# Performance work log

Measured on AMD Instinct MI355X. Metric: run time of the kernel, lower is better.

## Reference

```python
import jax, jax.numpy as jnp
import numpy as np

N = 100000   # nodes
S = 2        # layout samples per graph
G = 8        # graphs in batch
E = 400000   # directed edges
MID = 256    # mid_ch
L = 4        # n_layer
CLN = 2      # concat_last_n
IN_CH = 53 + 32 + 6 * 23 + 6 * 3 + 6 * 4  # 265


def setup_inputs() -> dict:
    key = jax.random.key(0)
    ks = jax.random.split(key, 16)
    f = lambda k, sh: jax.random.normal(k, sh, dtype=jnp.float32)
    return {
        "x_feat": f(ks[0], (N, 53)),
        "dim_feat": f(ks[1], (N, 6, 23)),
        "layout_feat": f(ks[2], (N, S, 6, 4)),
        "tile_feat": f(ks[3], (G, S, 6, 3)),
        "opcode_embed": f(ks[4], (121, 32)) * 0.02,
        "preW": f(ks[5], (IN_CH, MID)) * 0.05,
        "preb": jnp.zeros((MID,), jnp.float32),
        "convWl": f(ks[6], (L, MID, MID // 2)) * 0.05,
        "convWr": f(ks[7], (L, MID, MID // 2)) * 0.05,
        "convb": jnp.zeros((L, MID // 2), jnp.float32),
        "revWl": f(ks[8], (L, MID, MID // 2)) * 0.05,
        "revWr": f(ks[9], (L, MID, MID // 2)) * 0.05,
        "revb": jnp.zeros((L, MID // 2), jnp.float32),
        "headW": f(ks[10], (MID * CLN, 1)) * 0.05,
        "headb": jnp.zeros((1,), jnp.float32),
        "node_opcode": jax.random.randint(ks[11], (N,), 0, 121),
        "batch": jnp.sort(jax.random.randint(ks[12], (N,), 0, G)),
        "edge_index": jax.random.randint(ks[13], (2, E), 0, N),
    }


def _sage(x, src, tgt, inv_deg, Wl, Wr, b):
    # PyG SAGEConv: out = lin_l(mean_{j->i} x_j) + lin_r(x_i) + bias
    # x: [S, N, C]; gather messages from src, scatter-add into tgt.
    agg = jnp.zeros_like(x).at[:, tgt].add(x[:, src])
    agg = agg * inv_deg[None, :, None]
    return (jnp.einsum('snc,co->sno', agg, Wl)
            + jnp.einsum('snc,co->sno', x, Wr) + b)


def reference(x_feat, dim_feat, layout_feat, tile_feat, opcode_embed,
              preW, preb, convWl, convWr, convb, revWl, revWr, revb,
              headW, headb, node_opcode, batch, edge_index):
    op = opcode_embed[node_opcode]                       # [N, 32]
    base = jnp.concatenate([x_feat, op, dim_feat.reshape(N, -1)], axis=-1)
    x = jnp.concatenate([
        jnp.broadcast_to(base[None], (S,) + base.shape),          # [S,N,223]
        layout_feat.transpose(1, 0, 2, 3).reshape(S, N, -1),       # [S,N,24]
        tile_feat[batch].transpose(1, 0, 2, 3).reshape(S, N, -1),  # [S,N,18]
    ], axis=-1)                                                    # [S,N,265]
    x = jax.nn.relu(x @ preW + preb)                               # [S,N,MID]

    src, tgt = edge_index[0], edge_index[1]
    one = jnp.ones((E,), x.dtype)
    inv_fwd = 1.0 / jnp.maximum(jnp.zeros((N,), x.dtype).at[tgt].add(one), 1.0)
    inv_rev = 1.0 / jnp.maximum(jnp.zeros((N,), x.dtype).at[src].add(one), 1.0)

    xs = []
    for i in range(L):
        x = jnp.concatenate([
            _sage(x, src, tgt, inv_fwd, convWl[i], convWr[i], convb[i]),
            _sage(x, tgt, src, inv_rev, revWl[i], revWr[i], revb[i]),
        ], axis=-1)
        x = jax.nn.relu(x)
        if i >= L - CLN:
            xs.append(x)
    x = jnp.concatenate(xs, axis=-1)                     # [S, N, MID*CLN]

    pooled = jnp.zeros((S, G, x.shape[-1]), x.dtype).at[:, batch].add(x)
    out = pooled @ headW + headb                         # [S, G, 1]
    return out.transpose(1, 0, 2)                        # [G, S, 1]
```

## Files before the change

kernel.cpp:

```cpp
#include <hip/hip_runtime.h>
#include <hip/hip_bf16.h>

#define N_NODES 100000
#define S_SAMP 2
#define G_GRAPH 8
#define E_EDGES 400000
#define NLAYER 4
#define IN_CH 265
#define KPRE 384
#define NRT64 ((N_NODES + 63) / 64)
#define NPAD (NRT64 * 64)
#define NGRP ((NRT64 + 7) / 8)
#define NB1 ((N_NODES + 1023) / 1024)

typedef unsigned short u16;
typedef unsigned int u32;
typedef short bf16x8 __attribute__((ext_vector_type(8)));
typedef float f32x4 __attribute__((ext_vector_type(4)));

__device__ __forceinline__ float b2f(u16 u) {
    union { u32 i; float f; } x; x.i = ((u32)u) << 16; return x.f;
}
__device__ __forceinline__ u16 f2b(float f) {
    __hip_bfloat16 h = __float2bfloat16(f);
    return *reinterpret_cast<u16*>(&h);
}

__device__ __forceinline__ void gl_lds16(const u16* g, u16* l) {
    __builtin_amdgcn_global_load_lds(
        (const __attribute__((address_space(1))) void*)g,
        (__attribute__((address_space(3))) void*)l, 16, 0, 0);
}

__global__ void build_xin_k(const float* __restrict__ xf,
                            const float* __restrict__ dimf,
                            const float* __restrict__ layf,
                            const float* __restrict__ tilef,
                            const float* __restrict__ opemb,
                            const int* __restrict__ opcode,
                            const int* __restrict__ batch,
                            int s, u16* __restrict__ xin) {
    int n = blockIdx.x;
    int opc = opcode[n];
    int g = batch[n];
    u16* row = xin + (size_t)n * KPRE;
    for (int c = threadIdx.x; c < KPRE; c += blockDim.x) {
        float v = 0.0f;
        if (c < 53)       v = xf[(size_t)n * 53 + c];
        else if (c < 85)  v = opemb[opc * 32 + (c - 53)];
        else if (c < 223) v = dimf[(size_t)n * 138 + (c - 85)];
        else if (c < 247) v = layf[((size_t)n * S_SAMP + s) * 24 + (c - 223)];
        else if (c < 265) v = tilef[((size_t)g * S_SAMP + s) * 18 + (c - 247)];
        row[c] = f2b(v);
    }
}

__global__ void pack_w_k(const float* __restrict__ cWl, const float* __restrict__ rWl,
                         const float* __restrict__ cWr, const float* __restrict__ rWr,
                         const float* __restrict__ cb,  const float* __restrict__ rb,
                         u16* __restrict__ Wt, float* __restrict__ bcat) {
    int idx = blockIdx.x * blockDim.x + threadIdx.x;
    if (idx < NLAYER * 512 * 256) {
        int l = idx >> 17;
        int r = idx & 131071;
        int j = r >> 8;
        int k = r & 255;
        int jj = j & 255;
        int half = j >> 8;
        int sub = jj >> 7;
        int col = jj & 127;
        const float* src = half ? (sub ? rWl : cWl) : (sub ? rWr : cWr);
        Wt[idx] = f2b(src[((size_t)l * 256 + k) * 128 + col]);
    }
    if (idx < NLAYER * 512) {
        int l = idx >> 9;
        int j = idx & 511;
        float v = 0.0f;
        if (j < 256) v = (j < 128) ? cb[l * 128 + j] : rb[l * 128 + (j - 128)];
        bcat[idx] = v;
    }
}

__global__ void pack_pre_k(const float* __restrict__ preW, u16* __restrict__ preWt) {
    int idx = blockIdx.x * blockDim.x + threadIdx.x;
    if (idx >= 256 * KPRE) return;
    int j = idx / KPRE;
    int k = idx - j * KPRE;
    preWt[idx] = (k < IN_CH) ? f2b(preW[(size_t)k * 256 + j]) : (u16)0;
}

__global__ void deg_k(const int* __restrict__ ei, int* __restrict__ degF,
                      int* __restrict__ degR) {
    int e = blockIdx.x * blockDim.x + threadIdx.x;
    if (e < E_EDGES) {
        atomicAdd(&degF[ei[E_EDGES + e]], 1);
        atomicAdd(&degR[ei[e]], 1);
    }
}

__global__ __launch_bounds__(1024) void scan1_k(const int* __restrict__ degF,
                                                const int* __restrict__ degR,
                                                int* __restrict__ rpF,
                                                int* __restrict__ rpR,
                                                int* __restrict__ bsum) {
    const int* deg = blockIdx.y ? degR : degF;
    int* rp = blockIdx.y ? rpR : rpF;
    __shared__ int buf[1024];
    int i = blockIdx.x * 1024 + threadIdx.x;
    int v = (i < N_NODES) ? deg[i] : 0;
    buf[threadIdx.x] = v;
    __syncthreads();
    for (int off = 1; off < 1024; off <<= 1) {
        int t = (threadIdx.x >= off) ? buf[threadIdx.x - off] : 0;
        __syncthreads();
        buf[threadIdx.x] += t;
        __syncthreads();
    }
    if (i < N_NODES) rp[i] = buf[threadIdx.x] - v;
    if (threadIdx.x == 1023) bsum[blockIdx.y * NB1 + blockIdx.x] = buf[1023];
}

__global__ __launch_bounds__(256) void scan2_k(int* __restrict__ bsum,
                                               int* __restrict__ rpF,
                                               int* __restrict__ rpR) {
    __shared__ int buf[2][128];
    int half = threadIdx.x >> 7;
    int t = threadIdx.x & 127;
    int v = (t < NB1) ? bsum[half * NB1 + t] : 0;
    buf[half][t] = v;
    __syncthreads();
    for (int off = 1; off < 128; off <<= 1) {
        int x = (t >= off) ? buf[half][t - off] : 0;
        __syncthreads();
        buf[half][t] += x;
        __syncthreads();
    }
    if (t < NB1) bsum[half * NB1 + t] = buf[half][t] - v;
    if (t == NB1) (half ? rpR : rpF)[N_NODES] = buf[half][NB1 - 1];
}

__global__ void scan3_k(const int* __restrict__ bsum, int* __restrict__ rpF,
                        int* __restrict__ rpR) {
    int* rp = blockIdx.y ? rpR : rpF;
    int i = blockIdx.x * 1024 + threadIdx.x;
    if (i < N_NODES) rp[i] += bsum[blockIdx.y * NB1 + blockIdx.x];
}

__global__ void inv_cursor_k(const int* __restrict__ degF, const int* __restrict__ degR,
                             const int* __restrict__ rpF, const int* __restrict__ rpR,
                             float* __restrict__ invF, float* __restrict__ invR,
                             int* __restrict__ curF, int* __restrict__ curR) {
    int i = blockIdx.x * blockDim.x + threadIdx.x;
    if (i < N_NODES) {
        invF[i] = 1.0f / fmaxf((float)degF[i], 1.0f);
        invR[i] = 1.0f / fmaxf((float)degR[i], 1.0f);
        curF[i] = rpF[i];
        curR[i] = rpR[i];
    }
}

__global__ void fill_k(const int* __restrict__ ei, int* __restrict__ curF,
                       int* __restrict__ curR, int* __restrict__ colF,
                       int* __restrict__ colR) {
    int e = blockIdx.x * blockDim.x + threadIdx.x;
    if (e < E_EDGES) {
        int s = ei[e], t = ei[E_EDGES + e];
        colF[atomicAdd(&curF[t], 1)] = s;
        colR[atomicAdd(&curR[s], 1)] = t;
    }
}

template <bool RELU_OUT, int NCHUNK, int COLT>
__global__ __launch_bounds__(256) void mmA_k(const u16* __restrict__ A,
                                             const u16* __restrict__ Bt,
                                             const float* __restrict__ bias,
                                             u16* __restrict__ C0,
                                             u16* __restrict__ C1) {
    __shared__ u16 As[64 * 128];
    __shared__ u16 Bs[64 * 128];
    constexpr int K = NCHUNK * 128;

    int bid = blockIdx.x;
    int x = bid & 7;
    int q = bid >> 3;
    int c = q % COLT;
    int g = q / COLT;
    int rowTile = g * 8 + x;
    if (rowTile >= NRT64) return;
    int rowBase = rowTile * 64;
    int colBase = c * 64;

    int tid = threadIdx.x;
    int wv = tid >> 6;
    int lane = tid & 63;
    int quad = lane >> 4;
    int l16 = lane & 15;

    int rsub = lane >> 4;
    int sl = lane & 15;

    f32x4 acc[4] = {};

    for (int ci = 0; ci < NCHUNK; ci++) {
        int k0 = ci * 128;
        #pragma unroll
        for (int i = 0; i < 4; i++) {
            int r = wv * 16 + 4 * i + rsub;
            int ch = sl ^ (r & 15);
            gl_lds16(A + (size_t)(rowBase + r) * K + k0 + ch * 8,
                     As + (wv * 16 + 4 * i) * 128);
            gl_lds16(Bt + (size_t)(colBase + r) * K + k0 + ch * 8,
                     Bs + (wv * 16 + 4 * i) * 128);
        }
        __syncthreads();
        int ra = wv * 16 + l16;
        #pragma unroll
        for (int ks = 0; ks < 4; ks++) {
            int ca = ks * 4 + quad;
            bf16x8 af = *(const bf16x8*)(As + ra * 128 + (ca ^ (ra & 15)) * 8);
            #pragma unroll
            for (int cf = 0; cf < 4; cf++) {
                int rb = cf * 16 + l16;
                bf16x8 bf = *(const bf16x8*)(Bs + rb * 128 + (ca ^ (rb & 15)) * 8);
                acc[cf] = __builtin_amdgcn_mfma_f32_16x16x32_bf16(af, bf, acc[cf], 0, 0, 0);
            }
        }
        if (ci + 1 < NCHUNK) __syncthreads();
    }

    u16* dst = (colBase < 256) ? C0 : C1;
    int cb = colBase & 255;
    #pragma unroll
    for (int cf = 0; cf < 4; cf++) {
        int col = cb + cf * 16 + l16;
        float bv = bias[colBase + cf * 16 + l16];
        #pragma unroll
        for (int r = 0; r < 4; r++) {
            int row = rowBase + wv * 16 + quad * 4 + r;
            if (row < N_NODES) {
                float v = acc[cf][r] + bv;
                if (RELU_OUT) v = fmaxf(v, 0.0f);
                dst[(size_t)row * 256 + col] = f2b(v);
            }
        }
    }
}

template <bool DOT>
__global__ __launch_bounds__(256) void agg_k(const int* __restrict__ rpF,
                                             const int* __restrict__ colF,
                                             const int* __restrict__ rpR,
                                             const int* __restrict__ colR,
                                             const float* __restrict__ invF,
                                             const float* __restrict__ invR,
                                             const u16* __restrict__ H,
                                             u16* __restrict__ Xn,
                                             const float* __restrict__ w,
                                             float* __restrict__ dotbuf) {
    int n = (blockIdx.x * blockDim.x + threadIdx.x) >> 6;
    if (n >= N_NODES) return;
    int lane = threadIdx.x & 63;
    int half = lane >> 5;
    int l32 = lane & 31;
    const int* rp  = half ? rpR : rpF;
    const int* col = half ? colR : colF;
    float inv = half ? invR[n] : invF[n];
    const u16* Hb = H + half * 128 + 4 * l32;

    float a0 = 0, a1 = 0, a2 = 0, a3 = 0;
    int b = rp[n], e = rp[n + 1];
    int j = b;
    for (; j + 7 < e; j += 8) {
        int c0 = col[j],     c1 = col[j + 1], c2 = col[j + 2], c3 = col[j + 3];
        int c4 = col[j + 4], c5 = col[j + 5], c6 = col[j + 6], c7 = col[j + 7];
        ushort4 h0 = *(const ushort4*)(Hb + (size_t)c0 * 256);
        ushort4 h1 = *(const ushort4*)(Hb + (size_t)c1 * 256);
        ushort4 h2 = *(const ushort4*)(Hb + (size_t)c2 * 256);
        ushort4 h3 = *(const ushort4*)(Hb + (size_t)c3 * 256);
        ushort4 h4 = *(const ushort4*)(Hb + (size_t)c4 * 256);
        ushort4 h5 = *(const ushort4*)(Hb + (size_t)c5 * 256);
        ushort4 h6 = *(const ushort4*)(Hb + (size_t)c6 * 256);
        ushort4 h7 = *(const ushort4*)(Hb + (size_t)c7 * 256);
        a0 += b2f(h0.x) + b2f(h1.x) + b2f(h2.x) + b2f(h3.x)
            + b2f(h4.x) + b2f(h5.x) + b2f(h6.x) + b2f(h7.x);
        a1 += b2f(h0.y) + b2f(h1.y) + b2f(h2.y) + b2f(h3.y)
            + b2f(h4.y) + b2f(h5.y) + b2f(h6.y) + b2f(h7.y);
        a2 += b2f(h0.z) + b2f(h1.z) + b2f(h2.z) + b2f(h3.z)
            + b2f(h4.z) + b2f(h5.z) + b2f(h6.z) + b2f(h7.z);
        a3 += b2f(h0.w) + b2f(h1.w) + b2f(h2.w) + b2f(h3.w)
            + b2f(h4.w) + b2f(h5.w) + b2f(h6.w) + b2f(h7.w);
    }
    for (; j + 3 < e; j += 4) {
        int c0 = col[j], c1 = col[j + 1], c2 = col[j + 2], c3 = col[j + 3];
        ushort4 h0 = *(const ushort4*)(Hb + (size_t)c0 * 256);
        ushort4 h1 = *(const ushort4*)(Hb + (size_t)c1 * 256);
        ushort4 h2 = *(const ushort4*)(Hb + (size_t)c2 * 256);
        ushort4 h3 = *(const ushort4*)(Hb + (size_t)c3 * 256);
        a0 += b2f(h0.x) + b2f(h1.x) + b2f(h2.x) + b2f(h3.x);
        a1 += b2f(h0.y) + b2f(h1.y) + b2f(h2.y) + b2f(h3.y);
        a2 += b2f(h0.z) + b2f(h1.z) + b2f(h2.z) + b2f(h3.z);
        a3 += b2f(h0.w) + b2f(h1.w) + b2f(h2.w) + b2f(h3.w);
    }
    for (; j < e; j++) {
        int c = col[j];
        ushort4 h = *(const ushort4*)(Hb + (size_t)c * 256);
        a0 += b2f(h.x); a1 += b2f(h.y); a2 += b2f(h.z); a3 += b2f(h.w);
    }
    u16* xp = Xn + (size_t)n * 256 + 4 * lane;
    ushort4 xv = *(const ushort4*)xp;
    float v0 = fmaxf(b2f(xv.x) + a0 * inv, 0.0f);
    float v1 = fmaxf(b2f(xv.y) + a1 * inv, 0.0f);
    float v2 = fmaxf(b2f(xv.z) + a2 * inv, 0.0f);
    float v3 = fmaxf(b2f(xv.w) + a3 * inv, 0.0f);
    ushort4 o;
    o.x = f2b(v0); o.y = f2b(v1); o.z = f2b(v2); o.w = f2b(v3);
    *(ushort4*)xp = o;
    if (DOT) {
        float4 wv4 = *(const float4*)(w + 4 * lane);
        float d = v0 * wv4.x + v1 * wv4.y + v2 * wv4.z + v3 * wv4.w;
        #pragma unroll
        for (int off = 32; off > 0; off >>= 1) d += __shfl_down(d, off);
        if (lane == 0) dotbuf[n] = d;
    }
}

__global__ void out_init_k(float* __restrict__ out, const float* __restrict__ headb) {
    int i = threadIdx.x;
    if (i < G_GRAPH * S_SAMP) out[i] = headb[0];
}

__global__ __launch_bounds__(256) void reduce_k(const float* __restrict__ dotbuf,
                                                const int* __restrict__ batch,
                                                float* __restrict__ out, int s) {
    __shared__ float part[G_GRAPH];
    if (threadIdx.x < G_GRAPH) part[threadIdx.x] = 0.0f;
    __syncthreads();
    for (int i = blockIdx.x * 256 + threadIdx.x; i < N_NODES; i += gridDim.x * 256)
        atomicAdd(&part[batch[i]], dotbuf[i]);
    __syncthreads();
    if (threadIdx.x < G_GRAPH)
        atomicAdd(&out[threadIdx.x * S_SAMP + s], part[threadIdx.x]);
}

extern "C" void kernel_launch(void* const* d_in, const int* in_sizes, int n_in,
                              void* d_out, int out_size, void* d_ws, size_t ws_size,
                              hipStream_t stream) {
    const float* x_feat      = (const float*)d_in[0];
    const float* dim_feat    = (const float*)d_in[1];
    const float* layout_feat = (const float*)d_in[2];
    const float* tile_feat   = (const float*)d_in[3];
    const float* opemb       = (const float*)d_in[4];
    const float* preW        = (const float*)d_in[5];
    const float* preb        = (const float*)d_in[6];
    const float* convWl      = (const float*)d_in[7];
    const float* convWr      = (const float*)d_in[8];
    const float* convb       = (const float*)d_in[9];
    const float* revWl       = (const float*)d_in[10];
    const float* revWr       = (const float*)d_in[11];
    const float* revb        = (const float*)d_in[12];
    const float* headW       = (const float*)d_in[13];
    const float* headb       = (const float*)d_in[14];
    const int*   node_opcode = (const int*)d_in[15];
    const int*   batch       = (const int*)d_in[16];
    const int*   edge_index  = (const int*)d_in[17];
    float* out = (float*)d_out;

    char* ws = (char*)d_ws;
    size_t off = 0;
    auto alloc = [&](size_t nbytes) {
        char* p = ws + off;
        off += (nbytes + 255) & ~(size_t)255;
        return p;
    };
    u16* XA    = (u16*)alloc((size_t)NPAD * 256 * 2);
    u16* XB    = (u16*)alloc((size_t)NPAD * 256 * 2);
    u16* XinH  = (u16*)alloc((size_t)NPAD * KPRE * 2);
    u16* Wt    = (u16*)alloc((size_t)NLAYER * 512 * 256 * 2);
    u16* preWt = (u16*)alloc((size_t)256 * KPRE * 2);
    float* bcat = (float*)alloc(NLAYER * 512 * 4);
    float* dotbuf = (float*)alloc((size_t)N_NODES * 4);
    int* degF  = (int*)alloc(N_NODES * 4);
    int* degR  = (int*)alloc(N_NODES * 4);
    int* rpF   = (int*)alloc((N_NODES + 1) * 4);
    int* rpR   = (int*)alloc((N_NODES + 1) * 4);
    int* curF  = (int*)alloc(N_NODES * 4);
    int* curR  = (int*)alloc(N_NODES * 4);
    int* colF  = (int*)alloc(E_EDGES * 4);
    int* colR  = (int*)alloc(E_EDGES * 4);
    int* bsum  = (int*)alloc(2 * NB1 * 4);
    float* invF = (float*)alloc(N_NODES * 4);
    float* invR = (float*)alloc(N_NODES * 4);

    hipMemsetAsync(degF, 0, N_NODES * 4, stream);
    hipMemsetAsync(degR, 0, N_NODES * 4, stream);

    pack_w_k<<<(NLAYER * 512 * 256 + 255) / 256, 256, 0, stream>>>(
        convWl, revWl, convWr, revWr, convb, revb, Wt, bcat);
    pack_pre_k<<<(256 * KPRE + 255) / 256, 256, 0, stream>>>(preW, preWt);
    deg_k<<<(E_EDGES + 255) / 256, 256, 0, stream>>>(edge_index, degF, degR);
    scan1_k<<<dim3(NB1, 2), 1024, 0, stream>>>(degF, degR, rpF, rpR, bsum);
    scan2_k<<<1, 256, 0, stream>>>(bsum, rpF, rpR);
    scan3_k<<<dim3(NB1, 2), 1024, 0, stream>>>(bsum, rpF, rpR);
    inv_cursor_k<<<(N_NODES + 255) / 256, 256, 0, stream>>>(
        degF, degR, rpF, rpR, invF, invR, curF, curR);
    fill_k<<<(E_EDGES + 255) / 256, 256, 0, stream>>>(edge_index, curF, curR, colF, colR);

    out_init_k<<<1, 64, 0, stream>>>(out, headb);

    for (int s = 0; s < S_SAMP; s++) {
        build_xin_k<<<N_NODES, 256, 0, stream>>>(
            x_feat, dim_feat, layout_feat, tile_feat, opemb, node_opcode, batch, s, XinH);
        mmA_k<true, 3, 4><<<NGRP * 8 * 4, 256, 0, stream>>>(
            XinH, preWt, preb, XA, XA);

        u16* ins[NLAYER]  = {XA, XB, XA, XB};
        u16* outs[NLAYER] = {XB, XA, XB, XA};
        for (int l = 0; l < NLAYER; l++) {
            mmA_k<false, 2, 8><<<NGRP * 8 * 8, 256, 0, stream>>>(
                ins[l], Wt + (size_t)l * 512 * 256, bcat + (size_t)l * 512,
                outs[l], XinH);
            if (l < 2) {
                agg_k<false><<<(N_NODES * 64 + 255) / 256, 256, 0, stream>>>(
                    rpF, colF, rpR, colR, invF, invR, XinH, outs[l], nullptr, nullptr);
            } else {
                agg_k<true><<<(N_NODES * 64 + 255) / 256, 256, 0, stream>>>(
                    rpF, colF, rpR, colR, invF, invR, XinH, outs[l],
                    headW + (l == 2 ? 0 : 256), dotbuf);
                reduce_k<<<128, 256, 0, stream>>>(dotbuf, batch, out, s);
            }
        }
    }
}
```

Before: 1.504 ms.

## Merge both layout samples into single batched GEMM and aggregation passes

When the workspace is large enough, both samples are processed together. One input build writes the shared features plus each sample's layout and tile columns. A single pre-GEMM with 512 output columns uses a repacked weight so each column half yields one sample. All layer GEMMs, aggregations and reductions then run over 2N rows, halving the kernel launches and letting the graph gather reuse CSR reads across samples. The input build kernels are also vectorised to write four values per thread. The cost is more workspace, and the merged path only runs if ws_size reaches 330MB; otherwise the old per-sample path runs.

```diff
diff --git a/kernel.cpp b/kernel.cpp
--- a/kernel.cpp
+++ b/kernel.cpp
@@ -10,8 +10,9 @@
 #define KPRE 384
 #define NRT64 ((N_NODES + 63) / 64)
 #define NPAD (NRT64 * 64)
-#define NGRP ((NRT64 + 7) / 8)
 #define NB1 ((N_NODES + 1023) / 1024)
+#define M2 (S_SAMP * N_NODES)
+#define MT2 (M2 / 64)
 
 typedef unsigned short u16;
 typedef unsigned int u32;
@@ -32,27 +33,66 @@
         (__attribute__((address_space(3))) void*)l, 16, 0, 0);
 }
 
-__global__ void build_xin_k(const float* __restrict__ xf,
-                            const float* __restrict__ dimf,
-                            const float* __restrict__ layf,
-                            const float* __restrict__ tilef,
-                            const float* __restrict__ opemb,
-                            const int* __restrict__ opcode,
-                            const int* __restrict__ batch,
-                            int s, u16* __restrict__ xin) {
-    int n = blockIdx.x;
+__global__ __launch_bounds__(256) void build_m_k(const float* __restrict__ xf,
+                                                 const float* __restrict__ dimf,
+                                                 const float* __restrict__ layf,
+                                                 const float* __restrict__ tilef,
+                                                 const float* __restrict__ opemb,
+                                                 const int* __restrict__ opcode,
+                                                 const int* __restrict__ batch,
+                                                 u16* __restrict__ A2) {
+    int item = blockIdx.x * blockDim.x + threadIdx.x;
+    int n = item / 77;
+    if (n >= N_NODES) return;
+    int base = (item - n * 77) * 4;
     int opc = opcode[n];
     int g = batch[n];
-    u16* row = xin + (size_t)n * KPRE;
-    for (int c = threadIdx.x; c < KPRE; c += blockDim.x) {
+    ushort4 o;
+    u16* op = &o.x;
+    #pragma unroll
+    for (int u = 0; u < 4; u++) {
+        int c = base + u;
         float v = 0.0f;
         if (c < 53)       v = xf[(size_t)n * 53 + c];
         else if (c < 85)  v = opemb[opc * 32 + (c - 53)];
         else if (c < 223) v = dimf[(size_t)n * 138 + (c - 85)];
-        else if (c < 247) v = layf[((size_t)n * S_SAMP + s) * 24 + (c - 223)];
-        else if (c < 265) v = tilef[((size_t)g * S_SAMP + s) * 18 + (c - 247)];
-        row[c] = f2b(v);
-    }
+        else if (c < 247) v = layf[((size_t)n * 2 + 0) * 24 + (c - 223)];
+        else if (c < 265) v = tilef[((size_t)g * 2 + 0) * 18 + (c - 247)];
+        else if (c < 289) v = layf[((size_t)n * 2 + 1) * 24 + (c - 265)];
+        else if (c < 307) v = tilef[((size_t)g * 2 + 1) * 18 + (c - 289)];
+        op[u] = f2b(v);
+    }
+    *(ushort4*)(A2 + (size_t)n * KPRE + base) = o;
+}
+
+__global__ __launch_bounds__(256) void build_s_k(const float* __restrict__ xf,
+                                                 const float* __restrict__ dimf,
+                                                 const float* __restrict__ layf,
+                                                 const float* __restrict__ tilef,
+                                                 const float* __restrict__ opemb,
+                                                 const int* __restrict__ opcode,
+                                                 const int* __restrict__ batch,
+                                                 int s, u16* __restrict__ xin) {
+    int item = blockIdx.x * blockDim.x + threadIdx.x;
+    int n = item / 67;
+    if (n >= N_NODES) return;
+    int base = (item - n * 67) * 4;
+    int opc = opcode[n];
+    int g = batch[n];
+    ushort4 o;
+    u16* op = &o.x;
+    #pragma unroll
+    for (int u = 0; u < 4; u++) {
+        int c = base + u;
+        float v = 0.0f;
+        if (c < 53)       v = xf[(size_t)n * 53 + c];
+        else if (c < 85)  v = opemb[opc * 32 + (c - 53)];
+        else if (c < 223) v = dimf[(size_t)n * 138 + (c - 85)];
+        else if (c < 247) v = layf[((size_t)n * 2 + s) * 24 + (c - 223)];
+        else if (c < 265) v = tilef[((size_t)g * 2 + s) * 18 + (c - 247)];
+        op[u] = f2b(v);
+    }
+    *(ushort4*)(xin + (size_t)n * KPRE + base) = o;
 }
 
 __global__ void pack_w_k(const float* __restrict__ cWl, const float* __restrict__ rWl,
@@ -87,6 +127,26 @@
     int j = idx / KPRE;
     int k = idx - j * KPRE;
     preWt[idx] = (k < IN_CH) ? f2b(preW[(size_t)k * 256 + j]) : (u16)0;
+}
+
+__global__ void pack_pre2_k(const float* __restrict__ preW,
+                            const float* __restrict__ preb,
+                            u16* __restrict__ W2t, float* __restrict__ bias2) {
+    int idx = blockIdx.x * blockDim.x + threadIdx.x;
+    if (idx < 512 * KPRE) {
+        int j = idx / KPRE;
+        int k = idx - j * KPRE;
+        float v = 0.0f;
+        if (j < 256) {
+            if (k < IN_CH) v = preW[(size_t)k * 256 + j];
+        } else {
+            int jj = j - 256;
+            if (k < 223) v = preW[(size_t)k * 256 + jj];
+            else if (k >= 265 && k < 307) v = preW[(size_t)(k - 42) * 256 + jj];
+        }
+        W2t[idx] = f2b(v);
+    }
+    if (idx < 512) bias2[idx] = preb[idx & 255];
 }
 
 __global__ void deg_k(const int* __restrict__ ei, int* __restrict__ degF,
@@ -175,7 +235,8 @@
                                              const u16* __restrict__ Bt,
                                              const float* __restrict__ bias,
                                              u16* __restrict__ C0,
-                                             u16* __restrict__ C1) {
+                                             u16* __restrict__ C1,
+                                             int M, int Mtiles) {
     __shared__ u16 As[64 * 128];
     __shared__ u16 Bs[64 * 128];
     constexpr int K = NCHUNK * 128;
@@ -186,7 +247,7 @@
     int c = q % COLT;
     int g = q / COLT;
     int rowTile = g * 8 + x;
-    if (rowTile >= NRT64) return;
+    if (rowTile >= Mtiles) return;
     int rowBase = rowTile * 64;
     int colBase = c * 64;
 
@@ -195,7 +256,6 @@
     int lane = tid & 63;
     int quad = lane >> 4;
     int l16 = lane & 15;
-
     int rsub = lane >> 4;
     int sl = lane & 15;
 
@@ -237,7 +297,7 @@
         #pragma unroll
         for (int r = 0; r < 4; r++) {
             int row = rowBase + wv * 16 + quad * 4 + r;
-            if (row < N_NODES) {
+            if (row < M) {
                 float v = acc[cf][r] + bv;
                 if (RELU_OUT) v = fmaxf(v, 0.0f);
                 dst[(size_t)row * 256 + col] = f2b(v);
@@ -256,16 +316,19 @@
                                              const u16* __restrict__ H,
                                              u16* __restrict__ Xn,
                                              const float* __restrict__ w,
-                                             float* __restrict__ dotbuf) {
-    int n = (blockIdx.x * blockDim.x + threadIdx.x) >> 6;
-    if (n >= N_NODES) return;
+                                             float* __restrict__ dotbuf,
+                                             int nodes) {
+    int i = (blockIdx.x * blockDim.x + threadIdx.x) >> 6;
+    if (i >= nodes) return;
+    int s = (i >= N_NODES) ? 1 : 0;
+    int n = i - s * N_NODES;
     int lane = threadIdx.x & 63;
     int half = lane >> 5;
     int l32 = lane & 31;
     const int* rp  = half ? rpR : rpF;
     const int* col = half ? colR : colF;
     float inv = half ? invR[n] : invF[n];
-    const u16* Hb = H + half * 128 + 4 * l32;
+    const u16* Hb = H + ((size_t)s * N_NODES) * 256 + half * 128 + 4 * l32;
 
     float a0 = 0, a1 = 0, a2 = 0, a3 = 0;
     int b = rp[n], e = rp[n + 1];
@@ -306,7 +369,7 @@
         ushort4 h = *(const ushort4*)(Hb + (size_t)c * 256);
         a0 += b2f(h.x); a1 += b2f(h.y); a2 += b2f(h.z); a3 += b2f(h.w);
     }
-    u16* xp = Xn + (size_t)n * 256 + 4 * lane;
+    u16* xp = Xn + (size_t)i * 256 + 4 * lane;
     ushort4 xv = *(const ushort4*)xp;
     float v0 = fmaxf(b2f(xv.x) + a0 * inv, 0.0f);
     float v1 = fmaxf(b2f(xv.y) + a1 * inv, 0.0f);
@@ -320,7 +383,7 @@
         float d = v0 * wv4.x + v1 * wv4.y + v2 * wv4.z + v3 * wv4.w;
         #pragma unroll
         for (int off = 32; off > 0; off >>= 1) d += __shfl_down(d, off);
-        if (lane == 0) dotbuf[n] = d;
+        if (lane == 0) dotbuf[i] = d;
     }
 }
 
@@ -331,15 +394,19 @@
 
 __global__ __launch_bounds__(256) void reduce_k(const float* __restrict__ dotbuf,
                                                 const int* __restrict__ batch,
-                                                float* __restrict__ out, int s) {
-    __shared__ float part[G_GRAPH];
-    if (threadIdx.x < G_GRAPH) part[threadIdx.x] = 0.0f;
+                                                float* __restrict__ out,
+                                                int count, int s_base) {
+    __shared__ float part[G_GRAPH * S_SAMP];
+    if (threadIdx.x < G_GRAPH * S_SAMP) part[threadIdx.x] = 0.0f;
     __syncthreads();
-    for (int i = blockIdx.x * 256 + threadIdx.x; i < N_NODES; i += gridDim.x * 256)
-        atomicAdd(&part[batch[i]], dotbuf[i]);
+    for (int i = blockIdx.x * 256 + threadIdx.x; i < count; i += gridDim.x * 256) {
+        int s = s_base + ((i >= N_NODES) ? 1 : 0);
+        int n = (i >= N_NODES) ? i - N_NODES : i;
+        atomicAdd(&part[batch[n] * S_SAMP + s], dotbuf[i]);
+    }
     __syncthreads();
-    if (threadIdx.x < G_GRAPH)
-        atomicAdd(&out[threadIdx.x * S_SAMP + s], part[threadIdx.x]);
+    if (threadIdx.x < G_GRAPH * S_SAMP)
+        atomicAdd(&out[threadIdx.x], part[threadIdx.x]);
 }
 
 extern "C" void kernel_launch(void* const* d_in, const int* in_sizes, int n_in,
@@ -365,6 +432,8 @@
     const int*   edge_index  = (const int*)d_in[17];
     float* out = (float*)d_out;
 
+    const bool merged = ws_size >= (330ull << 20);
+
     char* ws = (char*)d_ws;
     size_t off = 0;
     auto alloc = [&](size_t nbytes) {
@@ -372,13 +441,16 @@
         off += (nbytes + 255) & ~(size_t)255;
         return p;
     };
-    u16* XA    = (u16*)alloc((size_t)NPAD * 256 * 2);
-    u16* XB    = (u16*)alloc((size_t)NPAD * 256 * 2);
-    u16* XinH  = (u16*)alloc((size_t)NPAD * KPRE * 2);
+    size_t xrows = merged ? (size_t)M2 : (size_t)NPAD;
+    u16* XA   = (u16*)alloc(xrows * 256 * 2);
+    u16* XB   = (u16*)alloc(xrows * 256 * 2);
+    u16* A2H  = (u16*)alloc(merged ? (size_t)M2 * 256 * 2 : (size_t)NPAD * KPRE * 2);
     u16* Wt    = (u16*)alloc((size_t)NLAYER * 512 * 256 * 2);
     u16* preWt = (u16*)alloc((size_t)256 * KPRE * 2);
-    float* bcat = (float*)alloc(NLAYER * 512 * 4);
-    float* dotbuf = (float*)alloc((size_t)N_NODES * 4);
+    u16* W2t   = (u16*)alloc((size_t)512 * KPRE * 2);
+    float* bcat  = (float*)alloc(NLAYER * 512 * 4);
+    float* bias2 = (float*)alloc(512 * 4);
+    float* dotbuf = (float*)alloc((merged ? M2 : N_NODES) * 4);
     int* degF  = (int*)alloc(N_NODES * 4);
     int* degR  = (int*)alloc(N_NODES * 4);
     int* rpF   = (int*)alloc((N_NODES + 1) * 4);
@@ -396,7 +468,6 @@
 
     pack_w_k<<<(NLAYER * 512 * 256 + 255) / 256, 256, 0, stream>>>(
         convWl, revWl, convWr, revWr, convb, revb, Wt, bcat);
-    pack_pre_k<<<(256 * KPRE + 255) / 256, 256, 0, stream>>>(preW, preWt);
     deg_k<<<(E_EDGES + 255) / 256, 256, 0, stream>>>(edge_index, degF, degR);
     scan1_k<<<dim3(NB1, 2), 1024, 0, stream>>>(degF, degR, rpF, rpR, bsum);
     scan2_k<<<1, 256, 0, stream>>>(bsum, rpF, rpR);
@@ -404,30 +475,63 @@
     inv_cursor_k<<<(N_NODES + 255) / 256, 256, 0, stream>>>(
         degF, degR, rpF, rpR, invF, invR, curF, curR);
     fill_k<<<(E_EDGES + 255) / 256, 256, 0, stream>>>(edge_index, curF, curR, colF, colR);
-
     out_init_k<<<1, 64, 0, stream>>>(out, headb);
 
-    for (int s = 0; s < S_SAMP; s++) {
-        build_xin_k<<<N_NODES, 256, 0, stream>>>(
-            x_feat, dim_feat, layout_feat, tile_feat, opemb, node_opcode, batch, s, XinH);
-        mmA_k<true, 3, 4><<<NGRP * 8 * 4, 256, 0, stream>>>(
-            XinH, preWt, preb, XA, XA);
-
+    if (merged) {
+        pack_pre2_k<<<(512 * KPRE + 255) / 256, 256, 0, stream>>>(preW, preb, W2t, bias2);
+        build_m_k<<<(N_NODES * 77 + 255) / 256, 256, 0, stream>>>(
+            x_feat, dim_feat, layout_feat, tile_feat, opemb, node_opcode, batch, A2H);
+        const int gridPre = ((NRT64 + 7) / 8) * 8 * 8;
+        mmA_k<true, 3, 8><<<gridPre, 256, 0, stream>>>(
+            A2H, W2t, bias2, XA, XA + (size_t)N_NODES * 256, N_NODES, NRT64);
+
+        const int gridL = ((MT2 + 7) / 8) * 8 * 8;
+        const int gridAgg = (M2 * 64 + 255) / 256;
         u16* ins[NLAYER]  = {XA, XB, XA, XB};
         u16* outs[NLAYER] = {XB, XA, XB, XA};
         for (int l = 0; l < NLAYER; l++) {
-            mmA_k<false, 2, 8><<<NGRP * 8 * 8, 256, 0, stream>>>(
+            mmA_k<false, 2, 8><<<gridL, 256, 0, stream>>>(
                 ins[l], Wt + (size_t)l * 512 * 256, bcat + (size_t)l * 512,
-                outs[l], XinH);
+                outs[l], A2H, M2, MT2);
             if (l < 2) {
-                agg_k<false><<<(N_NODES * 64 + 255) / 256, 256, 0, stream>>>(
-                    rpF, colF, rpR, colR, invF, invR, XinH, outs[l], nullptr, nullptr);
+                agg_k<false><<<gridAgg, 256, 0, stream>>>(
+                    rpF, colF, rpR, colR, invF, invR, A2H, outs[l],
+                    nullptr, nullptr, M2);
             } else {
-                agg_k<true><<<(N_NODES * 64 + 255) / 256, 256, 0, stream>>>(
-                    rpF, colF, rpR, colR, invF, invR, XinH, outs[l],
-                    headW + (l == 2 ? 0 : 256), dotbuf);
-                reduce_k<<<128, 256, 0, stream>>>(dotbuf, batch, out, s);
+                agg_k<true><<<gridAgg, 256, 0, stream>>>(
+                    rpF, colF, rpR, colR, invF, invR, A2H, outs[l],
+                    headW + (l == 2 ? 0 : 256), dotbuf, M2);
+                reduce_k<<<128, 256, 0, stream>>>(dotbuf, batch, out, M2, 0);
             }
         }
-    }
-}
+    } else {
+        pack_pre_k<<<(256 * KPRE + 255) / 256, 256, 0, stream>>>(preW, preWt);
+        const int gridPre = ((NRT64 + 7) / 8) * 8 * 4;
+        const int gridL   = ((NRT64 + 7) / 8) * 8 * 8;
+        const int gridAgg = (N_NODES * 64 + 255) / 256;
+        for (int s = 0; s < S_SAMP; s++) {
+            build_s_k<<<(N_NODES * 67 + 255) / 256, 256, 0, stream>>>(
+                x_feat, dim_feat, layout_feat, tile_feat, opemb, node_opcode,
+                batch, s, A2H);
+            mmA_k<true, 3, 4><<<gridPre, 256, 0, stream>>>(
+                A2H, preWt, preb, XA, XA, N_NODES, NRT64);
+            u16* ins[NLAYER]  = {XA, XB, XA, XB};
+            u16* outs[NLAYER] = {XB, XA, XB, XA};
+            for (int l = 0; l < NLAYER; l++) {
+                mmA_k<false, 2, 8><<<gridL, 256, 0, stream>>>(
+                    ins[l], Wt + (size_t)l * 512 * 256, bcat + (size_t)l * 512,
+                    outs[l], A2H, N_NODES, NRT64);
+                if (l < 2) {
+                    agg_k<false><<<gridAgg, 256, 0, stream>>>(
+                        rpF, colF, rpR, colR, invF, invR, A2H, outs[l],
+                        nullptr, nullptr, N_NODES);
+                } else {
+                    agg_k<true><<<gridAgg, 256, 0, stream>>>(
+                        rpF, colF, rpR, colR, invF, invR, A2H, outs[l],
+                        headW + (l == 2 ? 0 : 256), dotbuf, N_NODES);
+                    reduce_k<<<128, 256, 0, stream>>>(dotbuf, batch, out, N_NODES, s);
+                }
+            }
+        }
+    }
+}
```

Measured after the change: 1.458 ms. 1.03x faster.
